# Kernel tuning notes

Hardware: AMD Instinct MI355X
Metric: run time of the kernel (lower is better)

Reference implementation:

```python
import jax, jax.numpy as jnp
import numpy as np

THRESH = 0.3
DECAY = 0.5


def spike_fn(x):
    # Heaviside threshold (forward only)
    return (x > THRESH).astype(x.dtype)


def setup_inputs() -> dict:
    key = jax.random.key(0)
    k_in, k0, k1, k2 = jax.random.split(key, 4)
    B, D0, T = 128, 512, 512
    inputs = jax.random.uniform(k_in, (B, D0, T), dtype=jnp.float32)
    w0 = jax.random.normal(k0, (512, 1024), dtype=jnp.float32)
    w1 = jax.random.normal(k1, (1024, 1024), dtype=jnp.float32)
    w2 = jax.random.normal(k2, (1024, 512), dtype=jnp.float32)
    return {"inputs": inputs, "w0": w0, "w1": w1, "w2": w2}


def reference(inputs, w0, w1, w2):
    ws = (w0, w1, w2)
    B = inputs.shape[0]
    layer_dims = tuple(w.shape[1] for w in ws)

    # time-major: [T, B, D0]
    xs = jnp.transpose(inputs, (2, 0, 1))

    mem0 = tuple(jnp.zeros((B, d), dtype=inputs.dtype) for d in layer_dims)
    spk0 = tuple(jnp.zeros((B, d), dtype=inputs.dtype) for d in layer_dims)

    def step(carry, x_t):
        mems, spikes = carry
        prev_spike = x_t  # layer-0 spikes come straight from the input
        new_mems, new_spikes = [], []
        for i, w in enumerate(ws):
            # leaky integrate with reset-by-spike, then fire
            mem = mems[i] * DECAY * (1.0 - spikes[i]) + prev_spike @ w
            s = spike_fn(mem)
            new_mems.append(mem)
            new_spikes.append(s)
            prev_spike = s
        return (tuple(new_mems), tuple(new_spikes)), None

    (_, spikes_final), _ = jax.lax.scan(step, (mem0, spk0), xs)
    return spikes_final[-1]
```

## Files before the change

### kernel.cpp

```cpp
#include <hip/hip_runtime.h>


typedef __bf16 bf16;
typedef __attribute__((ext_vector_type(8))) __bf16 bf16x8;
typedef __attribute__((ext_vector_type(16))) float f32x16;
typedef unsigned long long u64;

#define B_   128
#define D0_  512
#define T_   512
#define TS_  128
#define N1_  1024
#define N2_  1024
#define N3_  512
#define MFMA32(a,b,c) __builtin_amdgcn_mfma_f32_32x32x16_bf16((a),(b),(c),0,0,0)

#define GL2LDS(g, l) __builtin_amdgcn_global_load_lds( \
    (const __attribute__((address_space(1))) void*)(g), \
    (__attribute__((address_space(3))) void*)(l), 16, 0, 0)

#define WAIT_BARRIER() do { \
    asm volatile("s_waitcnt vmcnt(0)" ::: "memory"); \
    __builtin_amdgcn_s_barrier(); } while (0)


__global__ __launch_bounds__(256)
void split_w(const float* __restrict__ W, bf16* __restrict__ WTh, bf16* __restrict__ WTl,
             int K, int N)
{
    __shared__ float tile[32][33];
    const int k0 = blockIdx.x * 32, n0 = blockIdx.y * 32;
    const int tx = threadIdx.x & 31, ty = threadIdx.x >> 5;
#pragma unroll
    for (int r = 0; r < 4; ++r)
        tile[ty + r * 8][tx] = W[(size_t)(k0 + ty + r * 8) * N + n0 + tx];
    __syncthreads();
#pragma unroll
    for (int r = 0; r < 4; ++r) {
        int nl = ty + r * 8;
        float v = tile[tx][nl];
        bf16 h = (bf16)v;
        size_t o = (size_t)(n0 + nl) * K + k0 + tx;
        WTh[o] = h;
        WTl[o] = (bf16)(v - (float)h);
    }
}

__global__ __launch_bounds__(256)
void split_x(const float* __restrict__ in, bf16* __restrict__ Xh, bf16* __restrict__ Xl)
{
    __shared__ float tile[32][33];
    const int b = blockIdx.z, d0 = blockIdx.x * 32, t0 = blockIdx.y * 32;
    const int tx = threadIdx.x & 31, ty = threadIdx.x >> 5;
#pragma unroll
    for (int r = 0; r < 4; ++r)
        tile[ty + r * 8][tx] = in[((size_t)b * D0_ + d0 + ty + r * 8) * T_ + t0 + tx];
    __syncthreads();
    const int s = t0 >> 7;
#pragma unroll
    for (int r = 0; r < 4; ++r) {
        int t  = t0 + ty + r * 8;
        int tl = t & (TS_ - 1);
        float v = tile[tx][ty + r * 8];
        bf16 h = (bf16)v;
        size_t o = (((size_t)s * B_ + b) * TS_ + tl) * D0_ + d0 + tx;
        Xh[o] = h;
        Xl[o] = (bf16)(v - (float)h);
    }
}

__device__ __forceinline__ bf16x8 expand8(unsigned v)
{
    union { unsigned u[4]; bf16x8 h; } r;
    const unsigned p = v * 0x8001u;
#pragma unroll
    for (int i = 0; i < 4; ++i)
        r.u[i] = ((p >> (2 * i)) & 0x10001u) * 0x3F80u;
    return r.h;
}

__global__ __launch_bounds__(256, 2)
void snn_layer0(const bf16* __restrict__ Ah, const bf16* __restrict__ Al,
                const bf16* __restrict__ WTh, const bf16* __restrict__ WTl,
                u64* __restrict__ bitsOut)
{
    constexpr int K = D0_;
    __shared__ char smem[65536];
    bf16* sA0  = (bf16*)(smem);
    bf16* sAl0 = (bf16*)(smem + 8192);
    bf16* sB0  = (bf16*)(smem + 16384);
    bf16* sBl0 = (bf16*)(smem + 24576);
    bf16* sA1  = (bf16*)(smem + 32768);
    bf16* sAl1 = (bf16*)(smem + 40960);
    bf16* sB1  = (bf16*)(smem + 49152);
    bf16* sBl1 = (bf16*)(smem + 57344);
    float* If  = (float*)smem;

    const int tid = threadIdx.x, lane = tid & 63, w = tid >> 6;
    const int wm = w & 1, wn = w >> 1;
    const int l31 = lane & 31, kh = lane >> 5;
    const int bid = blockIdx.x;
    const int b  = (bid & 7) | ((bid >> 6) << 3);
    const int nb = ((bid >> 3) & 7) * 128;

    const int i4 = lane >> 2, c4 = lane & 3;
    const int csrc = c4 ^ ((i4 >> 1) & 3);
    const bf16* gBh = WTh + (size_t)(nb + w * 32 + i4) * K + csrc * 8;
    const bf16* gBl = WTl + (size_t)(nb + w * 32 + i4) * K + csrc * 8;
    const int wT = w * 32 * 32;

    int rA[2], rB[2], swA[2], swB[2];
#pragma unroll
    for (int i = 0; i < 2; ++i) {
        rA[i] = wm * 64 + i * 32 + l31;
        rB[i] = wn * 64 + i * 32 + l31;
        swA[i] = (rA[i] >> 1) & 3;
        swB[i] = (rB[i] >> 1) & 3;
    }

    float cm = 0.f, cs = 0.f;
    const int scol = tid & 63;
    float* Ifb = If + (tid >> 6) * 4096;

#define STAGE0(dA, dAl, dBh, dBl, go)                                          \
    do {                                                                       \
        _Pragma("unroll")                                                      \
        for (int inst = 0; inst < 2; ++inst) {                                 \
            GL2LDS(gA  + (size_t)(inst * 16) * K + (go), (dA)  + wT + inst * 16 * 32); \
            GL2LDS(gAl + (size_t)(inst * 16) * K + (go), (dAl) + wT + inst * 16 * 32); \
            GL2LDS(gBh + (size_t)(inst * 16) * K + (go), (dBh) + wT + inst * 16 * 32); \
            GL2LDS(gBl + (size_t)(inst * 16) * K + (go), (dBl) + wT + inst * 16 * 32); \
        }                                                                      \
    } while (0)

#define KSTEP0(cA, cAl, cBh, cBl)                                              \
    do {                                                                       \
        bf16x8 a[2][2], al2[2][2];                                             \
        _Pragma("unroll")                                                      \
        for (int mi = 0; mi < 2; ++mi)                                         \
            _Pragma("unroll")                                                  \
            for (int h = 0; h < 2; ++h) {                                      \
                const int off = rA[mi] * 32 + (((2 * h + kh) ^ swA[mi]) * 8);  \
                a[mi][h]   = *(const bf16x8*)((cA) + off);                     \
                al2[mi][h] = *(const bf16x8*)((cAl) + off);                    \
            }                                                                  \
        _Pragma("unroll")                                                      \
        for (int h = 0; h < 2; ++h) {                                          \
            bf16x8 bh[2], bl[2];                                               \
            _Pragma("unroll")                                                  \
            for (int ni = 0; ni < 2; ++ni) {                                   \
                const int off = rB[ni] * 32 + (((2 * h + kh) ^ swB[ni]) * 8);  \
                bh[ni] = *(const bf16x8*)((cBh) + off);                        \
                bl[ni] = *(const bf16x8*)((cBl) + off);                        \
            }                                                                  \
            _Pragma("unroll")                                                  \
            for (int ni = 0; ni < 2; ++ni)                                     \
                _Pragma("unroll")                                              \
                for (int mi = 0; mi < 2; ++mi)                                 \
                    acc[mi][ni] = MFMA32(a[mi][h], bh[ni], acc[mi][ni]);       \
            _Pragma("unroll")                                                  \
            for (int ni = 0; ni < 2; ++ni)                                     \
                _Pragma("unroll")                                              \
                for (int mi = 0; mi < 2; ++mi)                                 \
                    acc[mi][ni] = MFMA32(al2[mi][h], bh[ni], acc[mi][ni]);     \
            _Pragma("unroll")                                                  \
            for (int ni = 0; ni < 2; ++ni)                                     \
                _Pragma("unroll")                                              \
                for (int mi = 0; mi < 2; ++mi)                                 \
                    acc[mi][ni] = MFMA32(a[mi][h], bl[ni], acc[mi][ni]);       \
        }                                                                      \
        WAIT_BARRIER();                                                        \
    } while (0)

#pragma unroll 1
    for (int s = 0; s < T_ / TS_; ++s) {
        const size_t arow = ((size_t)s * B_ + b) * TS_;
        const bf16* gA  = Ah + (arow + w * 32 + i4) * K + csrc * 8;
        const bf16* gAl = Al + (arow + w * 32 + i4) * K + csrc * 8;

        STAGE0(sA0, sAl0, sB0, sBl0, 0);
        WAIT_BARRIER();

        f32x16 acc[2][2] = {};

#pragma unroll 1
        for (int ks = 0; ks < K / 32; ks += 2) {
            STAGE0(sA1, sAl1, sB1, sBl1, (ks + 1) * 32);
            KSTEP0(sA0, sAl0, sB0, sBl0);
            if (ks + 2 < K / 32)
                STAGE0(sA0, sAl0, sB0, sBl0, (ks + 2) * 32);
            KSTEP0(sA1, sAl1, sB1, sBl1);
        }

        u64 word0 = 0, word1 = 0;
        if (wm == 0) {
#pragma unroll
            for (int ni = 0; ni < 2; ++ni)
#pragma unroll
                for (int mi = 0; mi < 2; ++mi)
#pragma unroll
                    for (int r = 0; r < 16; ++r) {
                        const int tt = mi * 32 + (r & 3) + 8 * (r >> 2) + 4 * kh;
                        If[wn * 4096 + tt * 64 + ni * 32 + l31] = acc[mi][ni][r];
                    }
        }
        __syncthreads();
        if (tid < 128) {
            float m = cm, sp = cs;
#pragma unroll 4
            for (int tt = 0; tt < 64; ++tt) {
                m = m * 0.5f * (1.0f - sp) + Ifb[tt * 64 + scol];
                const bool fire = m > 0.3f;
                sp = fire ? 1.0f : 0.0f;
                u64 bal = __ballot(fire);
                if ((tid & 63) == tt) word0 = bal;
            }
            cm = m; cs = sp;
        }
        __syncthreads();
        if (wm == 1) {
#pragma unroll
            for (int ni = 0; ni < 2; ++ni)
#pragma unroll
                for (int mi = 0; mi < 2; ++mi)
#pragma unroll
                    for (int r = 0; r < 16; ++r) {
                        const int tt = mi * 32 + (r & 3) + 8 * (r >> 2) + 4 * kh;
                        If[wn * 4096 + tt * 64 + ni * 32 + l31] = acc[mi][ni][r];
                    }
        }
        __syncthreads();
        if (tid < 128) {
            float m = cm, sp = cs;
#pragma unroll 4
            for (int tt = 0; tt < 64; ++tt) {
                m = m * 0.5f * (1.0f - sp) + Ifb[tt * 64 + scol];
                const bool fire = m > 0.3f;
                sp = fire ? 1.0f : 0.0f;
                u64 bal = __ballot(fire);
                if ((tid & 63) == tt) word1 = bal;
            }
            cm = m; cs = sp;
            u64* dst = bitsOut + ((size_t)s * B_ + b) * 2048;
            const int j8 = (nb >> 6) + (tid >> 6);
            const int t0 = tid & 63, t1 = 64 + (tid & 63);
            dst[t0 * 16 + (j8 ^ (t0 & 15))] = word0;
            dst[t1 * 16 + (j8 ^ (t1 & 15))] = word1;
        }
        __syncthreads();
    }
#undef STAGE0
#undef KSTEP0
}

template<bool WRITE_BITS>
__global__ __launch_bounds__(256, 2)
void snn_layer_bits(const u64* __restrict__ bitsIn,
                    const bf16* __restrict__ WTh, const bf16* __restrict__ WTl,
                    u64* __restrict__ bitsOut, float* __restrict__ outp, int N)
{
    constexpr int K = 1024;
    __shared__ char smem[81920];
    char* bitsLds = smem;
    bf16* sBh0 = (bf16*)(smem + 16384);
    bf16* sBl0 = (bf16*)(smem + 32768);
    bf16* sBh1 = (bf16*)(smem + 49152);
    bf16* sBl1 = (bf16*)(smem + 65536);
    float* If  = (float*)(smem + 16384);

    const int tid = threadIdx.x, lane = tid & 63, w = tid >> 6;
    const int wm = w & 1, wn = w >> 1;
    const int l31 = lane & 31, kh = lane >> 5;
    const int b = blockIdx.y;
    const int nb = blockIdx.x * 128;

    const int i8 = lane >> 3, c8 = lane & 7;
    const bf16* gBh = WTh + (size_t)(nb + w * 32 + i8) * K + (c8 ^ i8) * 8;
    const bf16* gBl = WTl + (size_t)(nb + w * 32 + i8) * K + (c8 ^ i8) * 8;
    const int wB = w * 32 * 64;

    int rA[2], rB[2];
#pragma unroll
    for (int i = 0; i < 2; ++i) {
        rA[i] = wm * 64 + i * 32 + l31;
        rB[i] = wn * 64 + i * 32 + l31;
    }
    const int sw7 = l31 & 7, sw15 = l31 & 15, sh8 = 8 * kh;

    float cm = 0.f, cs = 0.f;
    const int scol = tid & 63;
    float* Ifb = If + (tid >> 6) * 4096;

#define STAGEB(dBh, dBl, go)                                                   \
    do {                                                                       \
        _Pragma("unroll")                                                      \
        for (int inst = 0; inst < 4; ++inst) {                                 \
            GL2LDS(gBh + (size_t)(inst * 8) * K + (go), (dBh) + wB + inst * 8 * 64); \
            GL2LDS(gBl + (size_t)(inst * 8) * K + (go), (dBl) + wB + inst * 8 * 64); \
        }                                                                      \
    } while (0)

#define KSTEPB(ks, cBh, cBl)                                                   \
    do {                                                                       \
        u64 wA0 = *(const u64*)(bitsLds + rA[0] * 128 + (((ks) ^ sw15) << 3)) >> sh8; \
        u64 wA1 = *(const u64*)(bitsLds + rA[1] * 128 + (((ks) ^ sw15) << 3)) >> sh8; \
        _Pragma("unroll")                                                      \
        for (int h = 0; h < 4; ++h) {                                          \
            bf16x8 a0 = expand8((unsigned)(wA0 >> (16 * h)) & 0xFFu);          \
            bf16x8 a1 = expand8((unsigned)(wA1 >> (16 * h)) & 0xFFu);          \
            bf16x8 bh[2], bl[2];                                               \
            _Pragma("unroll")                                                  \
            for (int ni = 0; ni < 2; ++ni) {                                   \
                const int off = rB[ni] * 64 + (((2 * h + kh) ^ sw7) << 3);     \
                bh[ni] = *(const bf16x8*)((cBh) + off);                        \
                bl[ni] = *(const bf16x8*)((cBl) + off);                        \
            }                                                                  \
            acc[0][0] = MFMA32(a0, bh[0], acc[0][0]);                          \
            acc[1][0] = MFMA32(a1, bh[0], acc[1][0]);                          \
            acc[0][1] = MFMA32(a0, bh[1], acc[0][1]);                          \
            acc[1][1] = MFMA32(a1, bh[1], acc[1][1]);                          \
            acc[0][0] = MFMA32(a0, bl[0], acc[0][0]);                          \
            acc[1][0] = MFMA32(a1, bl[0], acc[1][0]);                          \
            acc[0][1] = MFMA32(a0, bl[1], acc[0][1]);                          \
            acc[1][1] = MFMA32(a1, bl[1], acc[1][1]);                          \
        }                                                                      \
        WAIT_BARRIER();                                                        \
    } while (0)

#pragma unroll 1
    for (int s = 0; s < T_ / TS_; ++s) {
        {
            const char* src = (const char*)bitsIn + ((size_t)s * B_ + b) * 16384;
#pragma unroll
            for (int i = 0; i < 4; ++i)
                GL2LDS(src + (w * 4 + i) * 1024 + lane * 16,
                       bitsLds + (w * 4 + i) * 1024);
        }
        STAGEB(sBh0, sBl0, 0);
        WAIT_BARRIER();

        f32x16 acc[2][2] = {};

#pragma unroll 1
        for (int ks = 0; ks < K / 64; ks += 2) {
            STAGEB(sBh1, sBl1, (ks + 1) * 64);
            KSTEPB(ks, sBh0, sBl0);
            if (ks + 2 < K / 64)
                STAGEB(sBh0, sBl0, (ks + 2) * 64);
            KSTEPB(ks + 1, sBh1, sBl1);
        }

        u64 word0 = 0, word1 = 0;
        if (wm == 0) {
#pragma unroll
            for (int ni = 0; ni < 2; ++ni)
#pragma unroll
                for (int mi = 0; mi < 2; ++mi)
#pragma unroll
                    for (int r = 0; r < 16; ++r) {
                        const int tt = mi * 32 + (r & 3) + 8 * (r >> 2) + 4 * kh;
                        If[wn * 4096 + tt * 64 + ni * 32 + l31] = acc[mi][ni][r];
                    }
        }
        __syncthreads();
        if (tid < 128) {
            float m = cm, sp = cs;
#pragma unroll 4
            for (int tt = 0; tt < 64; ++tt) {
                m = m * 0.5f * (1.0f - sp) + Ifb[tt * 64 + scol];
                const bool fire = m > 0.3f;
                sp = fire ? 1.0f : 0.0f;
                if constexpr (WRITE_BITS) {
                    u64 bal = __ballot(fire);
                    if ((tid & 63) == tt) word0 = bal;
                }
            }
            cm = m; cs = sp;
        }
        __syncthreads();
        if (wm == 1) {
#pragma unroll
            for (int ni = 0; ni < 2; ++ni)
#pragma unroll
                for (int mi = 0; mi < 2; ++mi)
#pragma unroll
                    for (int r = 0; r < 16; ++r) {
                        const int tt = mi * 32 + (r & 3) + 8 * (r >> 2) + 4 * kh;
                        If[wn * 4096 + tt * 64 + ni * 32 + l31] = acc[mi][ni][r];
                    }
        }
        __syncthreads();
        if (tid < 128) {
            float m = cm, sp = cs;
#pragma unroll 4
            for (int tt = 0; tt < 64; ++tt) {
                m = m * 0.5f * (1.0f - sp) + Ifb[tt * 64 + scol];
                const bool fire = m > 0.3f;
                sp = fire ? 1.0f : 0.0f;
                if constexpr (WRITE_BITS) {
                    u64 bal = __ballot(fire);
                    if ((tid & 63) == tt) word1 = bal;
                }
            }
            cm = m; cs = sp;
            if constexpr (WRITE_BITS) {
                u64* dst = bitsOut + ((size_t)s * B_ + b) * 2048;
                const int j8 = (nb >> 6) + (tid >> 6);
                const int t0 = tid & 63, t1 = 64 + (tid & 63);
                dst[t0 * 16 + (j8 ^ (t0 & 15))] = word0;
                dst[t1 * 16 + (j8 ^ (t1 & 15))] = word1;
            } else {
                if (s == T_ / TS_ - 1)
                    outp[(size_t)b * N + nb + tid] = cs;
            }
        }
        __syncthreads();
    }
#undef STAGEB
#undef KSTEPB
}

extern "C" void kernel_launch(void* const* d_in, const int* in_sizes, int n_in,
                              void* d_out, int out_size, void* d_ws, size_t ws_size,
                              hipStream_t stream)
{
    const float* x  = (const float*)d_in[0];
    const float* w0 = (const float*)d_in[1];
    const float* w1 = (const float*)d_in[2];
    const float* w2 = (const float*)d_in[3];
    float* out = (float*)d_out;

    char* p = (char*)d_ws;
    bf16* w0h = (bf16*)p;  p += (size_t)N1_ * D0_ * 2;
    bf16* w0l = (bf16*)p;  p += (size_t)N1_ * D0_ * 2;
    bf16* w1h = (bf16*)p;  p += (size_t)N2_ * N1_ * 2;
    bf16* w1l = (bf16*)p;  p += (size_t)N2_ * N1_ * 2;
    bf16* w2h = (bf16*)p;  p += (size_t)N3_ * N2_ * 2;
    bf16* w2l = (bf16*)p;  p += (size_t)N3_ * N2_ * 2;
    bf16* Xh  = (bf16*)p;  p += (size_t)T_ * B_ * D0_ * 2;
    bf16* Xl  = (bf16*)p;  p += (size_t)T_ * B_ * D0_ * 2;
    u64* bits0 = (u64*)p;  p += (size_t)(T_/TS_) * B_ * TS_ * (N1_/8);
    u64* bits1 = (u64*)p;  p += (size_t)(T_/TS_) * B_ * TS_ * (N2_/8);

    split_w<<<dim3(D0_/32, N1_/32), 256, 0, stream>>>(w0, w0h, w0l, D0_, N1_);
    split_w<<<dim3(N1_/32, N2_/32), 256, 0, stream>>>(w1, w1h, w1l, N1_, N2_);
    split_w<<<dim3(N2_/32, N3_/32), 256, 0, stream>>>(w2, w2h, w2l, N2_, N3_);
    split_x<<<dim3(D0_/32, T_/32, B_), 256, 0, stream>>>(x, Xh, Xl);

    snn_layer0<<<dim3(B_ * (N1_/128)), 256, 0, stream>>>(Xh, Xl, w0h, w0l, bits0);
    snn_layer_bits<true ><<<dim3(N2_/128, B_), 256, 0, stream>>>(
        bits0, w1h, w1l, bits1, nullptr, N2_);
    snn_layer_bits<false><<<dim3(N3_/128, B_), 256, 0, stream>>>(
        bits1, w2h, w2l, nullptr, out, N3_);
}
```

Before: 801.5 us.

## Use per-wave private B staging with vmcnt waits instead of block barriers

Restructures the snn_layer_bits main loop so each wave stages its own slice of the high/low weight tiles into a private LDS region, with 32-wide K steps. This replaces the per-k-step s_waitcnt+s_barrier with partial vmcnt(8) waits, so waves no longer synchronize with each other inside the GEMM loop. MFMA groups are bracketed with s_setprio, and the epilogue writes all accumulators at once and runs one 128-step recurrence instead of two 64-step halves. In exchange, pairs of waves (wm=0/1) now load the same B data twice, which doubles global-to-LDS traffic for B.

```diff
diff --git a/kernel.cpp b/kernel.cpp
--- a/kernel.cpp
+++ b/kernel.cpp
@@ -22,6 +22,9 @@
 #define WAIT_BARRIER() do { \
     asm volatile("s_waitcnt vmcnt(0)" ::: "memory"); \
     __builtin_amdgcn_s_barrier(); } while (0)
+
+#define VM8() asm volatile("s_waitcnt vmcnt(8)" ::: "memory")
+#define VM0() asm volatile("s_waitcnt vmcnt(0)" ::: "memory")
 
 
 __global__ __launch_bounds__(256)
@@ -262,11 +265,7 @@
     constexpr int K = 1024;
     __shared__ char smem[81920];
     char* bitsLds = smem;
-    bf16* sBh0 = (bf16*)(smem + 16384);
-    bf16* sBl0 = (bf16*)(smem + 32768);
-    bf16* sBh1 = (bf16*)(smem + 49152);
-    bf16* sBl1 = (bf16*)(smem + 65536);
-    float* If  = (float*)(smem + 16384);
+    float* If = (float*)(smem + 16384);
 
     const int tid = threadIdx.x, lane = tid & 63, w = tid >> 6;
     const int wm = w & 1, wn = w >> 1;
@@ -274,47 +273,46 @@
     const int b = blockIdx.y;
     const int nb = blockIdx.x * 128;
 
-    const int i8 = lane >> 3, c8 = lane & 7;
-    const bf16* gBh = WTh + (size_t)(nb + w * 32 + i8) * K + (c8 ^ i8) * 8;
-    const bf16* gBl = WTl + (size_t)(nb + w * 32 + i8) * K + (c8 ^ i8) * 8;
-    const int wB = w * 32 * 64;
-
-    int rA[2], rB[2];
-#pragma unroll
-    for (int i = 0; i < 2; ++i) {
-        rA[i] = wm * 64 + i * 32 + l31;
-        rB[i] = wn * 64 + i * 32 + l31;
-    }
-    const int sw7 = l31 & 7, sw15 = l31 & 15, sh8 = 8 * kh;
+    bf16* wbase = (bf16*)(smem + 16384 + w * 16384);
+
+    const int i4 = lane >> 2, c4 = lane & 3;
+    const int csrc = c4 ^ ((i4 >> 1) & 3);
+    const bf16* gBh = WTh + (size_t)(nb + wn * 64 + i4) * K + csrc * 8;
+    const bf16* gBl = WTl + (size_t)(nb + wn * 64 + i4) * K + csrc * 8;
+
+    const int sw3 = (l31 >> 1) & 3;
+    const int sh8 = 8 * kh;
+    const int rA0 = wm * 64 + l31, rA1 = wm * 64 + 32 + l31;
+    const int rA0b = rA0 * 128, rA1b = rA1 * 128;
+    const int s15 = l31 & 15;
 
     float cm = 0.f, cs = 0.f;
-    const int scol = tid & 63;
-    float* Ifb = If + (tid >> 6) * 4096;
-
-#define STAGEB(dBh, dBl, go)                                                   \
+
+#define STAGEP(j, go)                                                          \
     do {                                                                       \
         _Pragma("unroll")                                                      \
         for (int inst = 0; inst < 4; ++inst) {                                 \
-            GL2LDS(gBh + (size_t)(inst * 8) * K + (go), (dBh) + wB + inst * 8 * 64); \
-            GL2LDS(gBl + (size_t)(inst * 8) * K + (go), (dBl) + wB + inst * 8 * 64); \
+            GL2LDS(gBh + (size_t)(inst * 16) * K + (go), wbase + (j) * 4096 + inst * 512); \
+            GL2LDS(gBl + (size_t)(inst * 16) * K + (go), wbase + (j) * 4096 + 2048 + inst * 512); \
         }                                                                      \
     } while (0)
 
-#define KSTEPB(ks, cBh, cBl)                                                   \
+#define KSTEPP(j, x0, x1)                                                      \
     do {                                                                       \
-        u64 wA0 = *(const u64*)(bitsLds + rA[0] * 128 + (((ks) ^ sw15) << 3)) >> sh8; \
-        u64 wA1 = *(const u64*)(bitsLds + rA[1] * 128 + (((ks) ^ sw15) << 3)) >> sh8; \
+        const bf16* cBh = wbase + (j) * 4096;                                  \
+        const bf16* cBl = cBh + 2048;                                          \
         _Pragma("unroll")                                                      \
-        for (int h = 0; h < 4; ++h) {                                          \
-            bf16x8 a0 = expand8((unsigned)(wA0 >> (16 * h)) & 0xFFu);          \
-            bf16x8 a1 = expand8((unsigned)(wA1 >> (16 * h)) & 0xFFu);          \
+        for (int h = 0; h < 2; ++h) {                                          \
+            bf16x8 a0 = expand8(((x0) >> (16 * h + sh8)) & 0xFFu);             \
+            bf16x8 a1 = expand8(((x1) >> (16 * h + sh8)) & 0xFFu);             \
             bf16x8 bh[2], bl[2];                                               \
             _Pragma("unroll")                                                  \
             for (int ni = 0; ni < 2; ++ni) {                                   \
-                const int off = rB[ni] * 64 + (((2 * h + kh) ^ sw7) << 3);     \
-                bh[ni] = *(const bf16x8*)((cBh) + off);                        \
-                bl[ni] = *(const bf16x8*)((cBl) + off);                        \
+                const int off = (ni * 32 + l31) * 32 + (((2 * h + kh) ^ sw3) * 8); \
+                bh[ni] = *(const bf16x8*)(cBh + off);                          \
+                bl[ni] = *(const bf16x8*)(cBl + off);                          \
             }                                                                  \
+            __builtin_amdgcn_s_setprio(1);                                     \
             acc[0][0] = MFMA32(a0, bh[0], acc[0][0]);                          \
             acc[1][0] = MFMA32(a1, bh[0], acc[1][0]);                          \
             acc[0][1] = MFMA32(a0, bh[1], acc[0][1]);                          \
@@ -323,8 +321,8 @@
             acc[1][0] = MFMA32(a1, bl[0], acc[1][0]);                          \
             acc[0][1] = MFMA32(a0, bl[1], acc[0][1]);                          \
             acc[1][1] = MFMA32(a1, bl[1], acc[1][1]);                          \
+            __builtin_amdgcn_s_setprio(0);                                     \
         }                                                                      \
-        WAIT_BARRIER();                                                        \
     } while (0)
 
 #pragma unroll 1
@@ -336,70 +334,57 @@
                 GL2LDS(src + (w * 4 + i) * 1024 + lane * 16,
                        bitsLds + (w * 4 + i) * 1024);
         }
-        STAGEB(sBh0, sBl0, 0);
         WAIT_BARRIER();
+        STAGEP(0, 0);
 
         f32x16 acc[2][2] = {};
 
 #pragma unroll 1
-        for (int ks = 0; ks < K / 64; ks += 2) {
-            STAGEB(sBh1, sBl1, (ks + 1) * 64);
-            KSTEPB(ks, sBh0, sBl0);
-            if (ks + 2 < K / 64)
-                STAGEB(sBh0, sBl0, (ks + 2) * 64);
-            KSTEPB(ks + 1, sBh1, sBl1);
-        }
-
+        for (int ks = 0; ks < 30; ks += 2) {
+            const int pi = ks >> 1;
+            const u64 wa0 = *(const u64*)(bitsLds + rA0b + ((pi ^ s15) << 3));
+            const u64 wa1 = *(const u64*)(bitsLds + rA1b + ((pi ^ s15) << 3));
+            STAGEP(1, (ks + 1) * 32);
+            VM8();
+            KSTEPP(0, (unsigned)wa0, (unsigned)wa1);
+            STAGEP(0, (ks + 2) * 32);
+            VM8();
+            KSTEPP(1, (unsigned)(wa0 >> 32), (unsigned)(wa1 >> 32));
+        }
+        {
+            const u64 wa0 = *(const u64*)(bitsLds + rA0b + ((15 ^ s15) << 3));
+            const u64 wa1 = *(const u64*)(bitsLds + rA1b + ((15 ^ s15) << 3));
+            STAGEP(1, 31 * 32);
+            VM8();
+            KSTEPP(0, (unsigned)wa0, (unsigned)wa1);
+            VM0();
+            KSTEPP(1, (unsigned)(wa0 >> 32), (unsigned)(wa1 >> 32));
+        }
+
+        __syncthreads();
+#pragma unroll
+        for (int ni = 0; ni < 2; ++ni)
+#pragma unroll
+            for (int mi = 0; mi < 2; ++mi)
+#pragma unroll
+                for (int r = 0; r < 16; ++r) {
+                    const int tt = wm * 64 + mi * 32 + (r & 3) + 8 * (r >> 2) + 4 * kh;
+                    If[tt * 128 + wn * 64 + ni * 32 + l31] = acc[mi][ni][r];
+                }
+        __syncthreads();
         u64 word0 = 0, word1 = 0;
-        if (wm == 0) {
-#pragma unroll
-            for (int ni = 0; ni < 2; ++ni)
-#pragma unroll
-                for (int mi = 0; mi < 2; ++mi)
-#pragma unroll
-                    for (int r = 0; r < 16; ++r) {
-                        const int tt = mi * 32 + (r & 3) + 8 * (r >> 2) + 4 * kh;
-                        If[wn * 4096 + tt * 64 + ni * 32 + l31] = acc[mi][ni][r];
-                    }
-        }
-        __syncthreads();
         if (tid < 128) {
             float m = cm, sp = cs;
 #pragma unroll 4
-            for (int tt = 0; tt < 64; ++tt) {
-                m = m * 0.5f * (1.0f - sp) + Ifb[tt * 64 + scol];
+            for (int tt = 0; tt < 128; ++tt) {
+                m = m * 0.5f * (1.0f - sp) + If[tt * 128 + tid];
                 const bool fire = m > 0.3f;
                 sp = fire ? 1.0f : 0.0f;
                 if constexpr (WRITE_BITS) {
                     u64 bal = __ballot(fire);
-                    if ((tid & 63) == tt) word0 = bal;
-                }
-            }
-            cm = m; cs = sp;
-        }
-        __syncthreads();
-        if (wm == 1) {
-#pragma unroll
-            for (int ni = 0; ni < 2; ++ni)
-#pragma unroll
-                for (int mi = 0; mi < 2; ++mi)
-#pragma unroll
-                    for (int r = 0; r < 16; ++r) {
-                        const int tt = mi * 32 + (r & 3) + 8 * (r >> 2) + 4 * kh;
-                        If[wn * 4096 + tt * 64 + ni * 32 + l31] = acc[mi][ni][r];
+                    if ((tid & 63) == (tt & 63)) {
+                        if (tt < 64) word0 = bal; else word1 = bal;
                     }
-        }
-        __syncthreads();
-        if (tid < 128) {
-            float m = cm, sp = cs;
-#pragma unroll 4
-            for (int tt = 0; tt < 64; ++tt) {
-                m = m * 0.5f * (1.0f - sp) + Ifb[tt * 64 + scol];
-                const bool fire = m > 0.3f;
-                sp = fire ? 1.0f : 0.0f;
-                if constexpr (WRITE_BITS) {
-                    u64 bal = __ballot(fire);
-                    if ((tid & 63) == tt) word1 = bal;
                 }
             }
             cm = m; cs = sp;
@@ -416,8 +401,8 @@
         }
         __syncthreads();
     }
-#undef STAGEB
-#undef KSTEPB
+#undef STAGEP
+#undef KSTEPP
 }
 
 extern "C" void kernel_launch(void* const* d_in, const int* in_sizes, int n_in,
```

Measured after the change: 874.9 us. 1.09x slower.
